# Performance work log

Measured on AMD Instinct MI355X. Metric: run time of the kernel, lower is better.

## Reference

```python
import jax, jax.numpy as jnp
import numpy as np
from jax import lax

R = 128            # grid resolution (full-depth N3Tree equivalent)
BASIS = 9          # SH degree 2 -> 9 basis functions
DATA_DIM = 3 * BASIS + 1
B = 262144         # rays (512x512 image)
STEP_SIZE = 0.001
BG = 1.0           # background_brightness
NUM_STEPS = 256    # >= sqrt(3)*R worst-case voxel crossings

SH_C0 = 0.28209479177387814
SH_C1 = 0.4886025119029199
SH_C2 = (1.0925484305920792, -1.0925484305920792, 0.31539156525252005,
         -1.0925484305920792, 0.5462742152960396)


def eval_sh_bases(d):
    # d: [B,3] unit view directions -> [B,9] SH deg-2 basis values (matches svox.sh)
    x, y, z = d[:, 0], d[:, 1], d[:, 2]
    return jnp.stack([
        jnp.full_like(x, SH_C0),
        -SH_C1 * y,
        SH_C1 * z,
        -SH_C1 * x,
        SH_C2[0] * x * y,
        SH_C2[1] * y * z,
        SH_C2[2] * (2.0 * z * z - x * x - y * y),
        SH_C2[3] * x * z,
        SH_C2[4] * (x * x - y * y),
    ], axis=-1)


def dda_unit(cen, invdir):
    # slab intersection of ray (cen + t*dir) with unit cube [0,1]^3
    t1 = -cen * invdir            # [B,3]
    t2 = t1 + invdir
    tmin = jnp.maximum(jnp.max(jnp.minimum(t1, t2), axis=-1), 0.0)
    tmax = jnp.minimum(jnp.min(jnp.maximum(t1, t2), axis=-1), 1e9)
    return tmin, tmax


def setup_inputs() -> dict:
    key = jax.random.key(0)
    k1, k2, k3, k4 = jax.random.split(key, 4)
    origins = jax.random.uniform(k1, (B, 3), jnp.float32, 0.05, 0.95)
    dirs = jax.random.normal(k2, (B, 3), jnp.float32)
    viewdirs = jax.random.normal(k3, (B, 3), jnp.float32)
    viewdirs = viewdirs / jnp.linalg.norm(viewdirs, axis=-1, keepdims=True)
    tree_data = jax.random.normal(k4, (R, R, R, DATA_DIM), jnp.float32) * 0.5
    invradius = jnp.ones((3,), jnp.float32)
    return {"tree_data": tree_data, "origins": origins, "dirs": dirs,
            "viewdirs": viewdirs, "invradius": invradius}


def _render(tree_data, origins, dirs, viewdirs, invradius):
    nb = origins.shape[0]
    dirs = dirs / jnp.linalg.norm(dirs, axis=-1, keepdims=True)
    sh_mult = eval_sh_bases(viewdirs)[:, None, :]          # [B,1,9]
    invdirs = 1.0 / (dirs + 1e-9)
    t0, tmax = dda_unit(origins, invdirs)
    delta_scale = jnp.linalg.norm(dirs / invradius[None], axis=-1)  # [B]
    grid = tree_data.reshape(R * R * R, DATA_DIM)
    cube_sz = 1.0 / R

    def step(carry, _):
        t, light, out, active = carry
        pos = origins + t[:, None] * dirs                  # [B,3] in tree coords
        idx = jnp.clip(jnp.floor(pos * R), 0.0, R - 1.0)
        flat = (idx[:, 0] * (R * R) + idx[:, 1] * R + idx[:, 2]).astype(jnp.int32)
        rgba = grid[flat]                                  # [B,28] voxel query
        pos_t = pos * R - idx                              # local coords in voxel
        s0, s1 = dda_unit(pos_t, invdirs)
        dt = (s1 - s0) * cube_sz + STEP_SIZE
        sigma = jax.nn.relu(rgba[:, -1])
        att = jnp.exp(-dt * sigma * delta_scale)
        weight = light * (1.0 - att)
        rgb_sh = rgba[:, :-1].reshape(-1, 3, BASIS)
        rgb = jax.nn.sigmoid(jnp.sum(sh_mult * rgb_sh, axis=-1))  # [B,3]
        am = active[:, None]
        out = out + jnp.where(am, weight[:, None] * rgb, 0.0)
        light = jnp.where(active, light * att, light)
        t = t + jnp.where(active, dt, 0.0)
        active = active & (t < tmax)
        return (t, light, out, active), None

    init = (t0, jnp.ones((nb,), jnp.float32), jnp.zeros((nb, 3), jnp.float32),
            t0 < tmax)
    (t, light, out, active), _ = lax.scan(step, init, None, length=NUM_STEPS)
    # remaining transmittance hits background (white by default)
    return out + light[:, None] * BG


def reference(tree_data, origins, dirs, viewdirs, invradius):
    return _render(tree_data, origins, dirs, viewdirs, invradius)
```

## Files before the change

### kernel.cpp

```cpp
#include <hip/hip_runtime.h>
#include <hip/hip_fp16.h>
#include <math.h>

#define GRID_R 128
#define DATA_DIM 28
#define PAD_DIM 32
#define NSEG 8
#define SEG_STEPS 32
#define STEP_SIZE 0.001f
#define BG 1.0f

__device__ __forceinline__ float march_step(
    float t, float ox, float oy, float oz,
    float dx, float dy, float dz,
    float idx, float idy, float idz, int* flat)
{
    float px = (ox + t*dx) * 128.0f;
    float py = (oy + t*dy) * 128.0f;
    float pz = (oz + t*dz) * 128.0f;
    float fx = fminf(fmaxf(floorf(px), 0.0f), 127.0f);
    float fy = fminf(fmaxf(floorf(py), 0.0f), 127.0f);
    float fz = fminf(fmaxf(floorf(pz), 0.0f), 127.0f);
    *flat = (int)fx * (GRID_R*GRID_R) + (int)fy * GRID_R + (int)fz;
    float cx = px - fx, cy = py - fy, cz = pz - fz;
    float a1x = -cx*idx, a1y = -cy*idy, a1z = -cz*idz;
    float a2x = a1x+idx, a2y = a1y+idy, a2z = a1z+idz;
    float e1 = fminf(fminf(fmaxf(a1x,a2x), fmaxf(a1y,a2y)), fmaxf(a1z,a2z));
    e1 = fminf(e1, 1e9f);
    return e1 * (1.0f/128.0f) + STEP_SIZE;
}

#define RAY_SETUP(i)                                                          \
    float ox = origins[3*(i)+0], oy = origins[3*(i)+1], oz = origins[3*(i)+2];\
    float dx = dirs_in[3*(i)+0], dy = dirs_in[3*(i)+1], dz = dirs_in[3*(i)+2];\
    float dn = sqrtf(dx*dx + dy*dy + dz*dz);                                  \
    float rdn = 1.0f / dn;                                                    \
    dx *= rdn; dy *= rdn; dz *= rdn;                                          \
    float idx = 1.0f / (dx + 1e-9f);                                          \
    float idy = 1.0f / (dy + 1e-9f);                                          \
    float idz = 1.0f / (dz + 1e-9f);                                          \
    float t1x = -ox*idx, t1y = -oy*idy, t1z = -oz*idz;                        \
    float t2x = t1x+idx, t2y = t1y+idy, t2z = t1z+idz;                        \
    float t0   = fmaxf(fmaxf(fmaxf(fminf(t1x,t2x), fminf(t1y,t2y)), fminf(t1z,t2z)), 0.0f); \
    float tmax = fminf(fminf(fminf(fmaxf(t1x,t2x), fmaxf(t1y,t2y)), fmaxf(t1z,t2z)), 1e9f);

__global__ __launch_bounds__(256) void convert_kernel(
    const float* __restrict__ tree, __half* __restrict__ dst, int nvox)
{
    int tid = blockIdx.x * blockDim.x + threadIdx.x;
    int v = tid >> 2;
    int q = tid & 3;
    if (v >= nvox) return;
    const float* src = tree + (size_t)v * DATA_DIM + q * 8;
    float4 s0 = *(const float4*)(src);
    float4 s1 = make_float4(0.f, 0.f, 0.f, 0.f);
    if (q < 3) s1 = *(const float4*)(src + 4);
    union { uint4 u; __half2 h[4]; } w;
    w.h[0] = __floats2half2_rn(s0.x, s0.y);
    w.h[1] = __floats2half2_rn(s0.z, s0.w);
    w.h[2] = __floats2half2_rn(s1.x, s1.y);
    w.h[3] = __floats2half2_rn(s1.z, s1.w);
    *(uint4*)(dst + (size_t)v * PAD_DIM + q * 8) = w.u;
}

__global__ __launch_bounds__(256) void geom_kernel(
    const float* __restrict__ origins,
    const float* __restrict__ dirs_in,
    float* __restrict__ ckpt, int nB)
{
    int i = blockIdx.x * blockDim.x + threadIdx.x;
    if (i >= nB) return;
    RAY_SETUP(i);

    float ck[NSEG];
    float t = t0;
    ck[0] = t0;
#pragma unroll
    for (int k = 1; k < NSEG; ++k) {
        if (t < tmax) {
            for (int j = 0; j < SEG_STEPS; ++j) {
                int fl;
                t += march_step(t, ox, oy, oz, dx, dy, dz, idx, idy, idz, &fl);
                if (t >= tmax) break;
            }
        }
        ck[k] = t;
    }
    float* cp = ckpt + (size_t)i * NSEG;
    *(float4*)(cp + 0) = make_float4(ck[0], ck[1], ck[2], ck[3]);
    *(float4*)(cp + 4) = make_float4(ck[4], ck[5], ck[6], ck[7]);
}

__global__ __launch_bounds__(256, 8) void march_kernel(
    const __half* __restrict__ vox_grid,
    const float* __restrict__ origins,
    const float* __restrict__ dirs_in,
    const float* __restrict__ viewdirs,
    const float* __restrict__ invradius,
    const float* __restrict__ ckpt,
    float* __restrict__ out, int nB)
{
    int tid = blockIdx.x * blockDim.x + threadIdx.x;
    int ray = tid >> 3;
    int seg = tid & 7;
    if (ray >= nB) return;

    RAY_SETUP(ray);

    float vx = viewdirs[3*ray+0], vy = viewdirs[3*ray+1], vz = viewdirs[3*ray+2];
    float irx = invradius[0], iry = invradius[1], irz = invradius[2];
    float qx = dx / irx, qy = dy / iry, qz = dz / irz;
    float delta_scale = sqrtf(qx*qx + qy*qy + qz*qz);

    const float C0 = 0.28209479177387814f;
    const float C1 = 0.4886025119029199f;
    float sh0 = C0;
    float sh1 = -C1 * vy;
    float sh2 =  C1 * vz;
    float sh3 = -C1 * vx;
    float sh4 =  1.0925484305920792f  * vx * vy;
    float sh5 = -1.0925484305920792f * vy * vz;
    float sh6 =  0.31539156525252005f * (2.0f*vz*vz - vx*vx - vy*vy);
    float sh7 = -1.0925484305920792f * vx * vz;
    float sh8 =  0.5462742152960396f  * (vx*vx - vy*vy);

    float t = ckpt[(size_t)ray * NSEG + seg];
    float light = 1.0f;
    float o0 = 0.f, o1 = 0.f, o2 = 0.f;

    for (int j = 0; j < SEG_STEPS; ++j) {
        if (t >= tmax) break;
        int flat;
        float dt = march_step(t, ox, oy, oz, dx, dy, dz, idx, idy, idz, &flat);

        const uint4* vp = (const uint4*)(vox_grid + (size_t)flat * PAD_DIM);
        union { uint4 u[4]; __half2 h[16]; } rec;
        rec.u[0] = vp[0]; rec.u[1] = vp[1]; rec.u[2] = vp[2]; rec.u[3] = vp[3];

        float2 p0  = __half22float2(rec.h[0]);
        float2 p1  = __half22float2(rec.h[1]);
        float2 p2  = __half22float2(rec.h[2]);
        float2 p3  = __half22float2(rec.h[3]);
        float2 p4  = __half22float2(rec.h[4]);
        float2 p5  = __half22float2(rec.h[5]);
        float2 p6  = __half22float2(rec.h[6]);
        float2 p7  = __half22float2(rec.h[7]);
        float2 p8  = __half22float2(rec.h[8]);
        float2 p9  = __half22float2(rec.h[9]);
        float2 p10 = __half22float2(rec.h[10]);
        float2 p11 = __half22float2(rec.h[11]);
        float2 p12 = __half22float2(rec.h[12]);
        float2 p13 = __half22float2(rec.h[13]);

        float sigma = fmaxf(p13.y, 0.0f);
        float att = __expf(-dt * sigma * delta_scale);
        float weight = light * (1.0f - att);

        float r0 = sh0*p0.x + sh1*p0.y + sh2*p1.x + sh3*p1.y
                 + sh4*p2.x + sh5*p2.y + sh6*p3.x + sh7*p3.y + sh8*p4.x;
        float r1 = sh0*p4.y + sh1*p5.x + sh2*p5.y + sh3*p6.x
                 + sh4*p6.y + sh5*p7.x + sh6*p7.y + sh7*p8.x + sh8*p8.y;
        float r2 = sh0*p9.x + sh1*p9.y + sh2*p10.x + sh3*p10.y
                 + sh4*p11.x + sh5*p11.y + sh6*p12.x + sh7*p12.y + sh8*p13.x;

        float g0 = 1.0f / (1.0f + __expf(-r0));
        float g1 = 1.0f / (1.0f + __expf(-r1));
        float g2 = 1.0f / (1.0f + __expf(-r2));

        o0 += weight * g0;
        o1 += weight * g1;
        o2 += weight * g2;

        light *= att;
        t += dt;
    }

    float l0 = __shfl(light, 0, 8);
    float l1 = __shfl(light, 1, 8);
    float l2 = __shfl(light, 2, 8);
    float l3 = __shfl(light, 3, 8);
    float l4 = __shfl(light, 4, 8);
    float l5 = __shfl(light, 5, 8);
    float l6 = __shfl(light, 6, 8);
    float l7 = __shfl(light, 7, 8);

    float P = 1.0f;
    if (seg > 0) P *= l0;
    if (seg > 1) P *= l1;
    if (seg > 2) P *= l2;
    if (seg > 3) P *= l3;
    if (seg > 4) P *= l4;
    if (seg > 5) P *= l5;
    if (seg > 6) P *= l6;
    float total_light = l0*l1*l2*l3*l4*l5*l6*l7;

    o0 *= P; o1 *= P; o2 *= P;
    o0 += __shfl_xor(o0, 1, 8); o0 += __shfl_xor(o0, 2, 8); o0 += __shfl_xor(o0, 4, 8);
    o1 += __shfl_xor(o1, 1, 8); o1 += __shfl_xor(o1, 2, 8); o1 += __shfl_xor(o1, 4, 8);
    o2 += __shfl_xor(o2, 1, 8); o2 += __shfl_xor(o2, 2, 8); o2 += __shfl_xor(o2, 4, 8);

    if (seg == 0) {
        out[3*ray+0] = o0 + total_light * BG;
        out[3*ray+1] = o1 + total_light * BG;
        out[3*ray+2] = o2 + total_light * BG;
    }
}

extern "C" void kernel_launch(void* const* d_in, const int* in_sizes, int n_in,
                              void* d_out, int out_size, void* d_ws, size_t ws_size,
                              hipStream_t stream) {
    const float* tree      = (const float*)d_in[0];
    const float* origins   = (const float*)d_in[1];
    const float* dirs      = (const float*)d_in[2];
    const float* viewdirs  = (const float*)d_in[3];
    const float* invradius = (const float*)d_in[4];
    float* out = (float*)d_out;

    int nB   = in_sizes[1] / 3;
    int nvox = in_sizes[0] / DATA_DIM;

    const int block = 256;
    __half* hgrid = (__half*)d_ws;
    float* ckpt = (float*)((char*)d_ws + (size_t)nvox * PAD_DIM * sizeof(__half));

    int nconv = nvox * 4;
    convert_kernel<<<(nconv + block - 1) / block, block, 0, stream>>>(
        tree, hgrid, nvox);
    geom_kernel<<<(nB + block - 1) / block, block, 0, stream>>>(
        origins, dirs, ckpt, nB);
    int nmarch = nB * NSEG;
    march_kernel<<<(nmarch + block - 1) / block, block, 0, stream>>>(
        hgrid, origins, dirs, viewdirs, invradius, ckpt, out, nB);
    (void)ws_size;
}
```

Baseline: 725.7 us.

## Merge prep kernels, pack voxels for fdot2 SH dots, use native exp2/rcp

Merges the grid-conversion and checkpoint-geometry kernels into one launch that picks its role by block index. Each voxel's fp16 record is repacked with zero pads so the SH coefficients line up as half2 pairs. The march loop then computes the three SH dot products with v_dot2 fp16 instructions, using SH bases prescaled by log2(e). Sigmoid and attenuation switch to native exp2 and reciprocal, which saves conversions and ALU work per step but keeps the view-dependent SH weights only at fp16 precision.

```diff
diff --git a/kernel.cpp b/kernel.cpp
--- a/kernel.cpp
+++ b/kernel.cpp
@@ -9,6 +9,38 @@
 #define SEG_STEPS 32
 #define STEP_SIZE 0.001f
 #define BG 1.0f
+
+typedef _Float16 h2f __attribute__((ext_vector_type(2)));
+
+#if __has_builtin(__builtin_amdgcn_fdot2)
+__device__ __forceinline__ float fdot2(h2f a, h2f b, float c) {
+    return __builtin_amdgcn_fdot2(a, b, c, false);
+}
+#else
+__device__ __forceinline__ float fdot2(h2f a, h2f b, float c) {
+    return fmaf((float)a.x, (float)b.x, fmaf((float)a.y, (float)b.y, c));
+}
+#endif
+
+#if __has_builtin(__builtin_amdgcn_exp2f)
+__device__ __forceinline__ float fexp2(float x)    { return __builtin_amdgcn_exp2f(x); }
+__device__ __forceinline__ float fexp2neg(float x) { return __builtin_amdgcn_exp2f(-x); }
+#else
+__device__ __forceinline__ float fexp2(float x) {
+    float r; asm("v_exp_f32 %0, %1" : "=v"(r) : "v"(x)); return r;
+}
+__device__ __forceinline__ float fexp2neg(float x) {
+    float r; asm("v_exp_f32 %0, -%1" : "=v"(r) : "v"(x)); return r;
+}
+#endif
+
+#if __has_builtin(__builtin_amdgcn_rcpf)
+__device__ __forceinline__ float frcp(float x) { return __builtin_amdgcn_rcpf(x); }
+#else
+__device__ __forceinline__ float frcp(float x) {
+    float r; asm("v_rcp_f32 %0, %1" : "=v"(r) : "v"(x)); return r;
+}
+#endif
 
 __device__ __forceinline__ float march_step(
     float t, float ox, float oy, float oz,
@@ -21,7 +53,8 @@
     float fx = fminf(fmaxf(floorf(px), 0.0f), 127.0f);
     float fy = fminf(fmaxf(floorf(py), 0.0f), 127.0f);
     float fz = fminf(fmaxf(floorf(pz), 0.0f), 127.0f);
-    *flat = (int)fx * (GRID_R*GRID_R) + (int)fy * GRID_R + (int)fz;
+    float ff = fmaf(fx, 16384.0f, fmaf(fy, 128.0f, fz));
+    *flat = (int)ff;
     float cx = px - fx, cy = py - fy, cz = pz - fz;
     float a1x = -cx*idx, a1y = -cy*idy, a1z = -cz*idz;
     float a2x = a1x+idx, a2y = a1y+idy, a2z = a1z+idz;
@@ -44,51 +77,61 @@
     float t0   = fmaxf(fmaxf(fmaxf(fminf(t1x,t2x), fminf(t1y,t2y)), fminf(t1z,t2z)), 0.0f); \
     float tmax = fminf(fminf(fminf(fmaxf(t1x,t2x), fmaxf(t1y,t2y)), fmaxf(t1z,t2z)), 1e9f);
 
-__global__ __launch_bounds__(256) void convert_kernel(
-    const float* __restrict__ tree, __half* __restrict__ dst, int nvox)
+__global__ __launch_bounds__(256) void prep_kernel(
+    const float* __restrict__ tree, __half* __restrict__ vox, int nvox,
+    const float* __restrict__ origins, const float* __restrict__ dirs_in,
+    float* __restrict__ ckpt, int nB, int nGeomB)
 {
-    int tid = blockIdx.x * blockDim.x + threadIdx.x;
-    int v = tid >> 2;
-    int q = tid & 3;
-    if (v >= nvox) return;
-    const float* src = tree + (size_t)v * DATA_DIM + q * 8;
-    float4 s0 = *(const float4*)(src);
-    float4 s1 = make_float4(0.f, 0.f, 0.f, 0.f);
-    if (q < 3) s1 = *(const float4*)(src + 4);
-    union { uint4 u; __half2 h[4]; } w;
-    w.h[0] = __floats2half2_rn(s0.x, s0.y);
-    w.h[1] = __floats2half2_rn(s0.z, s0.w);
-    w.h[2] = __floats2half2_rn(s1.x, s1.y);
-    w.h[3] = __floats2half2_rn(s1.z, s1.w);
-    *(uint4*)(dst + (size_t)v * PAD_DIM + q * 8) = w.u;
-}
-
-__global__ __launch_bounds__(256) void geom_kernel(
-    const float* __restrict__ origins,
-    const float* __restrict__ dirs_in,
-    float* __restrict__ ckpt, int nB)
-{
-    int i = blockIdx.x * blockDim.x + threadIdx.x;
-    if (i >= nB) return;
-    RAY_SETUP(i);
-
-    float ck[NSEG];
-    float t = t0;
-    ck[0] = t0;
+    if ((int)blockIdx.x < nGeomB) {
+        int i = blockIdx.x * 256 + threadIdx.x;
+        if (i >= nB) return;
+        RAY_SETUP(i);
+        float ck[NSEG];
+        float t = t0;
+        ck[0] = t0;
 #pragma unroll
-    for (int k = 1; k < NSEG; ++k) {
-        if (t < tmax) {
-            for (int j = 0; j < SEG_STEPS; ++j) {
-                int fl;
-                t += march_step(t, ox, oy, oz, dx, dy, dz, idx, idy, idz, &fl);
-                if (t >= tmax) break;
+        for (int k = 1; k < NSEG; ++k) {
+            if (t < tmax) {
+                for (int j = 0; j < SEG_STEPS; ++j) {
+                    int fl;
+                    t += march_step(t, ox, oy, oz, dx, dy, dz, idx, idy, idz, &fl);
+                    if (t >= tmax) break;
+                }
             }
+            ck[k] = t;
         }
-        ck[k] = t;
+        float* cp = ckpt + (size_t)i * NSEG;
+        *(float4*)(cp + 0) = make_float4(ck[0], ck[1], ck[2], ck[3]);
+        *(float4*)(cp + 4) = make_float4(ck[4], ck[5], ck[6], ck[7]);
+    } else {
+        int v = (blockIdx.x - nGeomB) * 256 + threadIdx.x;
+        if (v >= nvox) return;
+        const float4* s4 = (const float4*)(tree + (size_t)v * DATA_DIM);
+        float4 A  = s4[0], B4 = s4[1], C4 = s4[2], D4 = s4[3],
+               E4 = s4[4], F4 = s4[5], G4 = s4[6];
+        uint4* d = (uint4*)(vox + (size_t)v * PAD_DIM);
+        union Q { __half2 h[4]; uint4 u; } q;
+        q.h[0] = __floats2half2_rn(A.x,  A.y);
+        q.h[1] = __floats2half2_rn(A.z,  A.w);
+        q.h[2] = __floats2half2_rn(B4.x, B4.y);
+        q.h[3] = __floats2half2_rn(B4.z, B4.w);
+        d[0] = q.u;
+        q.h[0] = __floats2half2_rn(C4.x, 0.f);
+        q.h[1] = __floats2half2_rn(C4.y, C4.z);
+        q.h[2] = __floats2half2_rn(C4.w, D4.x);
+        q.h[3] = __floats2half2_rn(D4.y, D4.z);
+        d[1] = q.u;
+        q.h[0] = __floats2half2_rn(D4.w, E4.x);
+        q.h[1] = __floats2half2_rn(E4.y, 0.f);
+        q.h[2] = __floats2half2_rn(E4.z, E4.w);
+        q.h[3] = __floats2half2_rn(F4.x, F4.y);
+        d[2] = q.u;
+        q.h[0] = __floats2half2_rn(F4.z, F4.w);
+        q.h[1] = __floats2half2_rn(G4.x, G4.y);
+        q.h[2] = __floats2half2_rn(G4.z, 0.f);
+        q.h[3] = __floats2half2_rn(G4.w, 0.f);
+        d[3] = q.u;
     }
-    float* cp = ckpt + (size_t)i * NSEG;
-    *(float4*)(cp + 0) = make_float4(ck[0], ck[1], ck[2], ck[3]);
-    *(float4*)(cp + 4) = make_float4(ck[4], ck[5], ck[6], ck[7]);
 }
 
 __global__ __launch_bounds__(256, 8) void march_kernel(
@@ -112,9 +155,9 @@
     float qx = dx / irx, qy = dy / iry, qz = dz / irz;
     float delta_scale = sqrtf(qx*qx + qy*qy + qz*qz);
 
-    const float C0 = 0.28209479177387814f;
     const float C1 = 0.4886025119029199f;
-    float sh0 = C0;
+    const float L2E = 1.4426950408889634f;
+    float sh0 = 0.28209479177387814f;
     float sh1 = -C1 * vy;
     float sh2 =  C1 * vz;
     float sh3 = -C1 * vx;
@@ -124,6 +167,13 @@
     float sh7 = -1.0925484305920792f * vx * vz;
     float sh8 =  0.5462742152960396f  * (vx*vx - vy*vy);
 
+    h2f S01 = { (_Float16)(sh0*L2E), (_Float16)(sh1*L2E) };
+    h2f S23 = { (_Float16)(sh2*L2E), (_Float16)(sh3*L2E) };
+    h2f S45 = { (_Float16)(sh4*L2E), (_Float16)(sh5*L2E) };
+    h2f S67 = { (_Float16)(sh6*L2E), (_Float16)(sh7*L2E) };
+    h2f S8z = { (_Float16)(sh8*L2E), (_Float16)0.0f      };
+    float nds = -delta_scale * L2E;
+
     float t = ckpt[(size_t)ray * NSEG + seg];
     float light = 1.0f;
     float o0 = 0.f, o1 = 0.f, o2 = 0.f;
@@ -134,44 +184,30 @@
         float dt = march_step(t, ox, oy, oz, dx, dy, dz, idx, idy, idz, &flat);
 
         const uint4* vp = (const uint4*)(vox_grid + (size_t)flat * PAD_DIM);
-        union { uint4 u[4]; __half2 h[16]; } rec;
+        union { uint4 u[4]; h2f h[16]; _Float16 s[32]; } rec;
         rec.u[0] = vp[0]; rec.u[1] = vp[1]; rec.u[2] = vp[2]; rec.u[3] = vp[3];
 
-        float2 p0  = __half22float2(rec.h[0]);
-        float2 p1  = __half22float2(rec.h[1]);
-        float2 p2  = __half22float2(rec.h[2]);
-        float2 p3  = __half22float2(rec.h[3]);
-        float2 p4  = __half22float2(rec.h[4]);
-        float2 p5  = __half22float2(rec.h[5]);
-        float2 p6  = __half22float2(rec.h[6]);
-        float2 p7  = __half22float2(rec.h[7]);
-        float2 p8  = __half22float2(rec.h[8]);
-        float2 p9  = __half22float2(rec.h[9]);
-        float2 p10 = __half22float2(rec.h[10]);
-        float2 p11 = __half22float2(rec.h[11]);
-        float2 p12 = __half22float2(rec.h[12]);
-        float2 p13 = __half22float2(rec.h[13]);
-
-        float sigma = fmaxf(p13.y, 0.0f);
-        float att = __expf(-dt * sigma * delta_scale);
-        float weight = light * (1.0f - att);
-
-        float r0 = sh0*p0.x + sh1*p0.y + sh2*p1.x + sh3*p1.y
-                 + sh4*p2.x + sh5*p2.y + sh6*p3.x + sh7*p3.y + sh8*p4.x;
-        float r1 = sh0*p4.y + sh1*p5.x + sh2*p5.y + sh3*p6.x
-                 + sh4*p6.y + sh5*p7.x + sh6*p7.y + sh7*p8.x + sh8*p8.y;
-        float r2 = sh0*p9.x + sh1*p9.y + sh2*p10.x + sh3*p10.y
-                 + sh4*p11.x + sh5*p11.y + sh6*p12.x + sh7*p12.y + sh8*p13.x;
-
-        float g0 = 1.0f / (1.0f + __expf(-r0));
-        float g1 = 1.0f / (1.0f + __expf(-r1));
-        float g2 = 1.0f / (1.0f + __expf(-r2));
-
-        o0 += weight * g0;
-        o1 += weight * g1;
-        o2 += weight * g2;
-
-        light *= att;
+        float sigma = fmaxf((float)rec.s[30], 0.0f);
+        float att = fexp2(dt * sigma * nds);
+        float la  = light * att;
+        float w   = light - la;
+        light = la;
+
+        float r0 = fdot2(rec.h[ 4], S8z, fdot2(rec.h[ 3], S67, fdot2(rec.h[ 2], S45,
+                   fdot2(rec.h[ 1], S23, fdot2(rec.h[ 0], S01, 0.0f)))));
+        float r1 = fdot2(rec.h[ 9], S8z, fdot2(rec.h[ 8], S67, fdot2(rec.h[ 7], S45,
+                   fdot2(rec.h[ 6], S23, fdot2(rec.h[ 5], S01, 0.0f)))));
+        float r2 = fdot2(rec.h[14], S8z, fdot2(rec.h[13], S67, fdot2(rec.h[12], S45,
+                   fdot2(rec.h[11], S23, fdot2(rec.h[10], S01, 0.0f)))));
+
+        float g0 = frcp(1.0f + fexp2neg(r0));
+        float g1 = frcp(1.0f + fexp2neg(r1));
+        float g2 = frcp(1.0f + fexp2neg(r2));
+
+        o0 = fmaf(w, g0, o0);
+        o1 = fmaf(w, g1, o1);
+        o2 = fmaf(w, g2, o2);
+
         t += dt;
     }
 
@@ -223,11 +259,11 @@
     __half* hgrid = (__half*)d_ws;
     float* ckpt = (float*)((char*)d_ws + (size_t)nvox * PAD_DIM * sizeof(__half));
 
-    int nconv = nvox * 4;
-    convert_kernel<<<(nconv + block - 1) / block, block, 0, stream>>>(
-        tree, hgrid, nvox);
-    geom_kernel<<<(nB + block - 1) / block, block, 0, stream>>>(
-        origins, dirs, ckpt, nB);
+    int nGeomB = (nB + block - 1) / block;
+    int nConvB = (nvox + block - 1) / block;
+    prep_kernel<<<nGeomB + nConvB, block, 0, stream>>>(
+        tree, hgrid, nvox, origins, dirs, ckpt, nB, nGeomB);
+
     int nmarch = nB * NSEG;
     march_kernel<<<(nmarch + block - 1) / block, block, 0, stream>>>(
         hgrid, origins, dirs, viewdirs, invradius, ckpt, out, nB);
```

After: 680.5 us. -6.2%, faster.
